# Kernel tuning notes

Hardware: AMD Instinct MI355X
Metric: run time of the kernel (lower is better)

## Reference

```python
import jax, jax.numpy as jnp
import numpy as np

NUM_EMBEDDINGS = 1024
EMBEDDING_DIM = 256
COMMITMENT_COST = 0.25
B, C, T = 16, 256, 4096


def setup_inputs() -> dict:
    key = jax.random.key(0)
    k_in, k_cb = jax.random.split(key)
    inputs = jax.random.normal(k_in, (B, C, T), dtype=jnp.float32)
    # matches nn.Embedding init uniform_(-1/K, 1/K)
    codebook = jax.random.uniform(
        k_cb, (NUM_EMBEDDINGS, EMBEDDING_DIM), dtype=jnp.float32,
        minval=-1.0 / NUM_EMBEDDINGS, maxval=1.0 / NUM_EMBEDDINGS)
    return {"inputs": inputs, "codebook": codebook}


def reference(inputs, codebook):
    # inputs: [B, C, T] -> [B, T, C] (channel-last), eval mode (no dead-code swap)
    x = jnp.transpose(inputs, (0, 2, 1))            # [B, T, C]
    flat = x.reshape(-1, EMBEDDING_DIM)             # [N, D]
    distances = (jnp.sum(flat * flat, axis=1, keepdims=True)
                 + jnp.sum(codebook * codebook, axis=1)
                 - 2.0 * jnp.matmul(flat, codebook.T))   # [N, K]
    encoding_indices = jnp.argmin(distances, axis=1)     # [N]
    quantized = codebook[encoding_indices].reshape(x.shape)  # [B, T, C]
    sg = jax.lax.stop_gradient
    e_latent_loss = jnp.mean(jnp.square(sg(quantized) - x))
    q_latent_loss = jnp.mean(jnp.square(quantized - sg(x)))
    vq_loss = e_latent_loss + COMMITMENT_COST * q_latent_loss
    quantized_st = x + sg(quantized - x)                 # straight-through
    quantized_st = jnp.transpose(quantized_st, (0, 2, 1))  # back to [B, C, T]
    indices = encoding_indices.reshape(B, T)
    return quantized_st, vq_loss, indices
```

## Files before the change

### kernel.cpp

```cpp
#include <hip/hip_runtime.h>
#include <stdint.h>

#define DIMS 256
#define NT 4096
#define NROWS 65536
#define THETA 1.5e-4f

typedef float    f32x4_t __attribute__((ext_vector_type(4)));
typedef _Float16 f16x8_t __attribute__((ext_vector_type(8)));
typedef _Float16 f16x4_t __attribute__((ext_vector_type(4)));

#define GLDS16(gsrc, ldst) \
  __builtin_amdgcn_global_load_lds((const __attribute__((address_space(1))) void*)(gsrc), \
      (__attribute__((address_space(3))) void*)(ldst), 16, 0, 0)

__global__ __launch_bounds__(64) void vq_prep(const float* __restrict__ cb,
                                              float* __restrict__ se,
                                              _Float16* __restrict__ cb16){
  __shared__ float sq[256];
  const int k = blockIdx.x;
  const int tid = threadIdx.x;
  float4 v = *(const float4*)(cb + (size_t)k*256 + tid*4);
  f16x4_t p;
  p.x = (_Float16)(v.x * 512.f);
  p.y = (_Float16)(v.y * 512.f);
  p.z = (_Float16)(v.z * 512.f);
  p.w = (_Float16)(v.w * 512.f);
  *(f16x4_t*)(cb16 + (size_t)k*256 + tid*4) = p;
  sq[tid*4+0] = __fmul_rn(v.x, v.x);
  sq[tid*4+1] = __fmul_rn(v.y, v.y);
  sq[tid*4+2] = __fmul_rn(v.z, v.z);
  sq[tid*4+3] = __fmul_rn(v.w, v.w);
  __syncthreads();
  if (tid < 16){
    const int h = tid >> 3, j = tid & 7;
    float r = sq[h*128 + j];
    #pragma unroll
    for (int i = 1; i < 16; ++i) r = __fadd_rn(r, sq[h*128 + j + 8*i]);
    r = __fadd_rn(r, __shfl_xor(r, 1));
    r = __fadd_rn(r, __shfl_xor(r, 2));
    r = __fadd_rn(r, __shfl_xor(r, 4));
    r = __fadd_rn(r, __shfl_xor(r, 8));
    if (tid == 0) se[k] = r;
  }
}


#define AH(r,c)    Ah[(size_t)(r)*264 + (c)]
#define QQ(t,c)    q[(size_t)(t)*260 + (c)]

#define T2I(v, i, v1, i1, v2) { \
  bool lt = (v) < (v1); \
  (v2) = lt ? (v1) : fminf((v2), (v)); \
  (i1) = lt ? (i) : (i1); \
  (v1) = lt ? (v) : (v1); }

#define DECL_T2(M,R) \
  float b1_##M##R = 3.4e38f, b2_##M##R = 3.4e38f; int bi_##M##R = 0x7fffffff;

#define FOLD(M,R) { \
  float v; \
  v = fmaf(a##M##0[R], NEGI, ec0); T2I(v, kb +  0, b1_##M##R, bi_##M##R, b2_##M##R); \
  v = fmaf(a##M##1[R], NEGI, ec1); T2I(v, kb + 16, b1_##M##R, bi_##M##R, b2_##M##R); \
  v = fmaf(a##M##2[R], NEGI, ec2); T2I(v, kb + 32, b1_##M##R, bi_##M##R, b2_##M##R); \
  v = fmaf(a##M##3[R], NEGI, ec3); T2I(v, kb + 48, b1_##M##R, bi_##M##R, b2_##M##R); }

#define MSTEP(MK) { \
  float ov1 = __shfl_xor(v1, MK); int oi1 = __shfl_xor(i1, MK); float ov2 = __shfl_xor(v2, MK); \
  bool tk = ov1 < v1; \
  v2 = tk ? fminf(v1, ov2) : fminf(v2, ov1); \
  i1 = tk ? oi1 : i1; \
  v1 = tk ? ov1 : v1; }

#define MERGE(M,R) { \
  float v1 = b1_##M##R, v2 = b2_##M##R; int i1 = bi_##M##R; \
  MSTEP(1) MSTEP(2) MSTEP(4) MSTEP(8) \
  if (fr == 0) comb[(wr32 + (M)*16 + fq*4 + (R))*4 + wc] = make_float4(v1, __int_as_float(i1), v2, 0.f); }

__global__ __launch_bounds__(512, 1) void vq_scores(
    const float* __restrict__ x, const float* __restrict__ cb,
    const _Float16* __restrict__ cb16, const float* __restrict__ se,
    float* __restrict__ out0, float* __restrict__ out2,
    unsigned* __restrict__ wl, unsigned* __restrict__ cnt, double* __restrict__ accd)
{
  __shared__ __align__(16) char smem[71168];
  _Float16* Ah   = (_Float16*)smem;
  char*     BhRaw= smem + 33792;
  float4*   comb = (float4*)(smem + 66560);
  int*      codeL= (int*)(smem + 70656);
  float*    sxa  = (float*)(smem + 70912);
  float*    q    = (float*)smem;

  const int tid  = threadIdx.x;
  const int lane = tid & 63;
  const int wid  = tid >> 6;
  const int wr   = wid >> 2;
  const int wc   = wid & 3;
  const int fr   = lane & 15;
  const int fq   = lane >> 4;
  const int wr32 = wr * 32;
  const int fq8  = fq * 8;
  const int wcfr = wc*64 + fr;
  const int n0   = blockIdx.x * 64;
  const int bb   = n0 >> 12;
  const int t0   = n0 & 4095;
  const float NEGI = -1.0f/256.0f;

  const int cA = wid*32 + (lane >> 2);
  const int cB = cA + 16;
  const int qA = (lane & 3) ^ ((cA >> 1) & 3);
  const int qB = (lane & 3) ^ ((cB >> 1) & 3);
  const char* cbB = (const char*)cb16;
  const size_t srcA = (size_t)cA*512 + qA*16;
  const size_t srcB = (size_t)cB*512 + qB*16;
  char* dstA = BhRaw + wid*2048;
  char* dstB = dstA + 1024;

  int bOff[4];
  #pragma unroll
  for (int cf = 0; cf < 4; ++cf){
    const int cd = wc*64 + cf*16 + fr;
    bOff[cf] = cd*64 + ((fq ^ ((cd >> 1) & 3)) << 4);
  }

  GLDS16(cbB + srcA, dstA);
  GLDS16(cbB + srcB, dstB);

  {
    const int dup = tid >> 7;
    const int c4  = tid & 7;
    const int tt  = ((tid >> 3) & 15) << 2;
    #pragma unroll
    for (int cc2 = 0; cc2 < 2; ++cc2){
      const int c0 = (dup*2 + cc2) * 32;
      const float* xp = x + ((size_t)(bb*DIMS + c0 + c4*4))*NT + t0 + tt;
      f32x4_t va0 = __builtin_nontemporal_load((const f32x4_t*)(xp));
      f32x4_t va1 = __builtin_nontemporal_load((const f32x4_t*)(xp + NT));
      f32x4_t va2 = __builtin_nontemporal_load((const f32x4_t*)(xp + 2*NT));
      f32x4_t va3 = __builtin_nontemporal_load((const f32x4_t*)(xp + 3*NT));
      #pragma unroll
      for (int j = 0; j < 4; ++j){
        f16x4_t p;
        p.x = (_Float16)(va0[j]);
        p.y = (_Float16)(va1[j]);
        p.z = (_Float16)(va2[j]);
        p.w = (_Float16)(va3[j]);
        *(f16x4_t*)&AH(tt + j, c0 + c4*4) = p;
      }
    }
  }
  comb[(tid >> 2)*4 + (tid & 3)] = make_float4(3.4e38f, __int_as_float(0x7fffffff), 3.4e38f, 0.f);

  const f32x4_t Z = {0.f, 0.f, 0.f, 0.f};
  f32x4_t a00=Z,a01=Z,a02=Z,a03=Z, a10=Z,a11=Z,a12=Z,a13=Z;
  DECL_T2(0,0) DECL_T2(0,1) DECL_T2(0,2) DECL_T2(0,3)
  DECL_T2(1,0) DECL_T2(1,1) DECL_T2(1,2) DECL_T2(1,3)

  __syncthreads();

  for (int p = 0; p < 32; ++p){
    if (p){
      asm volatile("s_waitcnt vmcnt(0)" ::: "memory");
      __builtin_amdgcn_s_barrier();
      asm volatile("" ::: "memory");
    }
    const int nn = p + 1;
    if (nn < 32){
      const char* g = cbB + (size_t)(nn >> 3)*131072 + (size_t)(nn & 7)*64;
      char* d = (nn & 1) ? (dstA + 16384) : dstA;
      GLDS16(g + srcA, d);
      GLDS16(g + srcB, d + 1024);
    }
    {
      const char* bbuf = BhRaw + ((p & 1) << 14);
      f16x8_t bh0 = *(const f16x8_t*)(bbuf + bOff[0]);
      f16x8_t bh1 = *(const f16x8_t*)(bbuf + bOff[1]);
      f16x8_t bh2 = *(const f16x8_t*)(bbuf + bOff[2]);
      f16x8_t bh3 = *(const f16x8_t*)(bbuf + bOff[3]);
      const int cc = p & 7;
      f16x8_t ah0 = *(const f16x8_t*)&AH(wr32 + fr, cc*32 + fq8);
      f16x8_t ah1 = *(const f16x8_t*)&AH(wr32 + 16 + fr, cc*32 + fq8);
      __builtin_amdgcn_s_setprio(1);
      a00 = __builtin_amdgcn_mfma_f32_16x16x32_f16(ah0, bh0, a00, 0, 0, 0);
      a01 = __builtin_amdgcn_mfma_f32_16x16x32_f16(ah0, bh1, a01, 0, 0, 0);
      a02 = __builtin_amdgcn_mfma_f32_16x16x32_f16(ah0, bh2, a02, 0, 0, 0);
      a03 = __builtin_amdgcn_mfma_f32_16x16x32_f16(ah0, bh3, a03, 0, 0, 0);
      a10 = __builtin_amdgcn_mfma_f32_16x16x32_f16(ah1, bh0, a10, 0, 0, 0);
      a11 = __builtin_amdgcn_mfma_f32_16x16x32_f16(ah1, bh1, a11, 0, 0, 0);
      a12 = __builtin_amdgcn_mfma_f32_16x16x32_f16(ah1, bh2, a12, 0, 0, 0);
      a13 = __builtin_amdgcn_mfma_f32_16x16x32_f16(ah1, bh3, a13, 0, 0, 0);
      __builtin_amdgcn_s_setprio(0);
    }
    if ((p & 7) == 7){
      const int kb = (p >> 3)*256 + wcfr;
      const float ec0 = se[kb], ec1 = se[kb+16], ec2 = se[kb+32], ec3 = se[kb+48];
      FOLD(0,0) FOLD(0,1) FOLD(0,2) FOLD(0,3)
      FOLD(1,0) FOLD(1,1) FOLD(1,2) FOLD(1,3)
      a00=Z;a01=Z;a02=Z;a03=Z; a10=Z;a11=Z;a12=Z;a13=Z;
    }
  }

  MERGE(0,0) MERGE(0,1) MERGE(0,2) MERGE(0,3)
  MERGE(1,0) MERGE(1,1) MERGE(1,2) MERGE(1,3)
  __syncthreads();

  {
    const int row = tid >> 3, seg = tid & 7;
    float s = 0.f;
    #pragma unroll
    for (int k = 0; k < 4; ++k){
      f16x8_t hv = *(const f16x8_t*)&AH(row, seg*32 + k*8);
      #pragma unroll
      for (int e = 0; e < 8; ++e){
        float f = (float)hv[e];
        s = fmaf(f, f, s);
      }
    }
    s += __shfl_xor(s, 1);
    s += __shfl_xor(s, 2);
    s += __shfl_xor(s, 4);
    if (seg == 0) sxa[row] = s;
  }
  __syncthreads();

  if (tid < 64){
    float4 pv = comb[tid*4 + 0];
    float v1 = pv.x, v2 = pv.z;
    int   i1 = __float_as_int(pv.y);
    #pragma unroll
    for (int w = 1; w < 4; ++w){
      pv = comb[tid*4 + w];
      bool tk = pv.x < v1;
      v2 = tk ? fminf(v1, pv.z) : fminf(v2, pv.x);
      i1 = tk ? __float_as_int(pv.y) : i1;
      v1 = tk ? pv.x : v1;
    }
    const int r = n0 + tid;
    codeL[tid] = i1;
    out2[r] = (float)i1;
    bool flg = !(v2 - v1 >= THETA);
    if (flg){
      unsigned pos = atomicAdd(cnt, 1u);
      wl[pos] = (unsigned)r;
    }
    double c = flg ? 0.0 : (double)(sxa[tid] + v1);
    #pragma unroll
    for (int m = 1; m < 64; m <<= 1) c += __shfl_xor(c, m);
    if (tid == 0) atomicAdd(accd, c);
  }
  __syncthreads();

  {
    const int r = tid >> 3, seg = tid & 7;
    const float* src = cb + (size_t)codeL[r] * DIMS;
    #pragma unroll
    for (int k = 0; k < 8; ++k){
      float4 v = *(const float4*)(src + k*32 + seg*4);
      *(float4*)&QQ(r, k*32 + seg*4) = v;
    }
  }
  __syncthreads();

  {
    #pragma unroll
    for (int jj = 0; jj < 2; ++jj){
      const int c = wid*32 + jj*16 + (lane >> 2);
      float* dst = out0 + ((size_t)(bb*256 + c))*NT + t0;
      #pragma unroll
      for (int ii = 0; ii < 4; ++ii){
        const int tl = ii*16 + (lane & 3)*4;
        f32x4_t v;
        v[0] = QQ(tl + 0, c);
        v[1] = QQ(tl + 1, c);
        v[2] = QQ(tl + 2, c);
        v[3] = QQ(tl + 3, c);
        __builtin_nontemporal_store(v, (f32x4_t*)(dst + tl));
      }
    }
  }
}

__global__ __launch_bounds__(256) void vq_refine(
    const float* __restrict__ x, const float* __restrict__ cb,
    const float* __restrict__ se,
    const unsigned* __restrict__ wl, const unsigned* __restrict__ cnt,
    float* __restrict__ out2, float* __restrict__ out0, double* __restrict__ accd)
{
  __shared__ float eT[8][1024];
  __shared__ float xs[DIMS][8];
  __shared__ int   rows_s[8];
  __shared__ float sxs[8];
  __shared__ float wv[4][8];
  __shared__ int   wi[4][8];
  __shared__ int   wiF[8];

  const unsigned n = *cnt;
  const unsigned groups = (n + 7u) >> 3;
  const int tid  = threadIdx.x;
  const int lane = tid & 63;
  const int wid  = tid >> 6;

  for (unsigned g = blockIdx.x; g < groups; g += gridDim.x){
    __syncthreads();
    if (tid < 8){
      unsigned e = g*8u + (unsigned)tid;
      rows_s[tid] = (int)wl[e < n ? e : (n - 1u)];
    }
    __syncthreads();
    #pragma unroll
    for (int rep = 0; rep < 8; ++rep){
      int id = rep * 256 + tid;
      int c = id >> 3, r = id & 7;
      int row = rows_s[r];
      xs[c][r] = x[((size_t)((row >> 12)*DIMS + c))*NT + (row & 4095)];
    }
    __syncthreads();
    if (tid < 128){
      const int r = tid >> 4, hj = tid & 15;
      const int h = hj >> 3, j = hj & 7;
      float v0 = xs[h*128 + j][r];
      float s = __fmul_rn(v0, v0);
      #pragma unroll
      for (int i = 1; i < 16; ++i){
        float v = xs[h*128 + j + 8*i][r];
        s = __fadd_rn(s, __fmul_rn(v, v));
      }
      s = __fadd_rn(s, __shfl_xor(s, 1));
      s = __fadd_rn(s, __shfl_xor(s, 2));
      s = __fadd_rn(s, __shfl_xor(s, 4));
      s = __fadd_rn(s, __shfl_xor(s, 8));
      if (hj == 0) sxs[r] = s;
    }

    float s[8][4];
    #pragma unroll
    for (int r = 0; r < 8; ++r)
      #pragma unroll
      for (int u = 0; u < 4; ++u) s[r][u] = 0.f;

    for (int c0 = 0; c0 < DIMS; c0 += 8){
      __syncthreads();
      #pragma unroll
      for (int rep = 0; rep < 8; ++rep){
        int id2 = rep * 256 + tid;
        int k = id2 >> 1, qq = id2 & 1;
        float4 v = *(const float4*)&cb[(size_t)k * DIMS + c0 + qq * 4];
        eT[qq*4 + 0][k] = v.x; eT[qq*4 + 1][k] = v.y;
        eT[qq*4 + 2][k] = v.z; eT[qq*4 + 3][k] = v.w;
      }
      __syncthreads();
      #pragma unroll
      for (int cc = 0; cc < 8; ++cc){
        float4 ev = *(const float4*)&eT[cc][wid*256 + lane*4];
        #pragma unroll
        for (int r = 0; r < 8; ++r){
          float xv = xs[c0 + cc][r];
          s[r][0] = fmaf(xv, ev.x, s[r][0]);
          s[r][1] = fmaf(xv, ev.y, s[r][1]);
          s[r][2] = fmaf(xv, ev.z, s[r][2]);
          s[r][3] = fmaf(xv, ev.w, s[r][3]);
        }
      }
    }

    float4 sek = *(const float4*)&se[wid*256 + lane*4];
    #pragma unroll
    for (int r = 0; r < 8; ++r){
      const float sxv = sxs[r];
      float bv = 3.4e38f; int bi = 0x7fffffff;
      #pragma unroll
      for (int u = 0; u < 4; ++u){
        float d = __fsub_rn(__fadd_rn(sxv, (&sek.x)[u]),
                            __fadd_rn(s[r][u], s[r][u]));
        int k = wid*256 + lane*4 + u;
        if (d < bv || (d == bv && k < bi)) { bv = d; bi = k; }
      }
      #pragma unroll
      for (int m = 1; m < 64; m <<= 1){
        float ov = __shfl_xor(bv, m);
        int   oi = __shfl_xor(bi, m);
        if (ov < bv || (ov == bv && oi < bi)) { bv = ov; bi = oi; }
      }
      if (lane == 0){ wv[wid][r] = bv; wi[wid][r] = bi; }
    }
    __syncthreads();
    if (tid < 8){
      const int r = tid;
      float bv = wv[0][r]; int bi = wi[0][r];
      #pragma unroll
      for (int w = 1; w < 4; ++w){
        float ov = wv[w][r]; int oi = wi[w][r];
        if (ov < bv || (ov == bv && oi < bi)) { bv = ov; bi = oi; }
      }
      wiF[r] = bi;
      if (g*8u + (unsigned)r < n){
        int row = rows_s[r];
        out2[row] = (float)bi;
        atomicAdd(accd, (double)bv);
      }
    }
    __syncthreads();
    #pragma unroll
    for (int r = 0; r < 8; ++r){
      if (g*8u + (unsigned)r < n){
        int row  = rows_s[r];
        int code = wiF[r];
        out0[((size_t)((row >> 12)*256 + tid))*NT + (row & 4095)] = cb[(size_t)code*DIMS + tid];
      }
    }
  }
}

__global__ void vq_final(const double* __restrict__ accd, float* __restrict__ out1){
  *out1 = (float)(1.25 * (*accd) * (1.0 / 16777216.0));
}

extern "C" void kernel_launch(void* const* d_in, const int* in_sizes, int n_in,
                              void* d_out, int out_size, void* d_ws, size_t ws_size,
                              hipStream_t stream)
{
  const float* x  = (const float*)d_in[0];
  const float* cb = (const float*)d_in[1];
  float* out  = (float*)d_out;
  float* out0 = out;
  float* out1 = out + (size_t)16777216;
  float* out2 = out + (size_t)16777217;

  char* ws = (char*)d_ws;
  double*   accd = (double*)(ws + 0);
  unsigned* cnt  = (unsigned*)(ws + 8);
  float*    se   = (float*)(ws + 64);
  unsigned* wl   = (unsigned*)(ws + 4160);
  _Float16* cb16 = (_Float16*)(ws + 266304);

  hipMemsetAsync(d_ws, 0, 16, stream);
  vq_prep  <<<dim3(1024), dim3(64),  0, stream>>>(cb, se, cb16);
  vq_scores<<<dim3(1024), dim3(512), 0, stream>>>(x, cb, cb16, se, out0, out2, wl, cnt, accd);
  vq_refine<<<dim3(512),  dim3(256), 0, stream>>>(x, cb, se, wl, cnt, out2, out0, accd);
  vq_final <<<dim3(1),    dim3(1),   0, stream>>>(accd, out1);
}
```

Baseline: 159.6 us.

## Track top-3 candidates and resolve two-way ties with a cheap pair-refine kernel

```diff
diff --git a/kernel.cpp b/kernel.cpp
--- a/kernel.cpp
+++ b/kernel.cpp
@@ -45,50 +45,68 @@
   }
 }
 
-
 #define AH(r,c)    Ah[(size_t)(r)*264 + (c)]
 #define QQ(t,c)    q[(size_t)(t)*260 + (c)]
 
-#define T2I(v, i, v1, i1, v2) { \
-  bool lt = (v) < (v1); \
-  (v2) = lt ? (v1) : fminf((v2), (v)); \
-  (i1) = lt ? (i) : (i1); \
-  (v1) = lt ? (v) : (v1); }
-
-#define DECL_T2(M,R) \
-  float b1_##M##R = 3.4e38f, b2_##M##R = 3.4e38f; int bi_##M##R = 0x7fffffff;
+#define T3I(v, i, V1, I1, V2, I2, V3) { \
+  bool lt1 = (v) < (V1), lt2 = (v) < (V2), lt3 = (v) < (V3); \
+  (V3) = lt2 ? (V2) : (lt3 ? (v) : (V3)); \
+  (V2) = lt1 ? (V1) : (lt2 ? (v) : (V2)); \
+  (I2) = lt1 ? (I1) : (lt2 ? (i) : (I2)); \
+  (V1) = lt1 ? (v) : (V1); \
+  (I1) = lt1 ? (i) : (I1); }
+
+#define DECL_T3(M,R) \
+  float b1_##M##R = 3.4e38f, b2_##M##R = 3.4e38f, b3_##M##R = 3.4e38f; \
+  int bi_##M##R = 0x7fffffff, bj_##M##R = 0x7fffffff;
 
 #define FOLD(M,R) { \
   float v; \
-  v = fmaf(a##M##0[R], NEGI, ec0); T2I(v, kb +  0, b1_##M##R, bi_##M##R, b2_##M##R); \
-  v = fmaf(a##M##1[R], NEGI, ec1); T2I(v, kb + 16, b1_##M##R, bi_##M##R, b2_##M##R); \
-  v = fmaf(a##M##2[R], NEGI, ec2); T2I(v, kb + 32, b1_##M##R, bi_##M##R, b2_##M##R); \
-  v = fmaf(a##M##3[R], NEGI, ec3); T2I(v, kb + 48, b1_##M##R, bi_##M##R, b2_##M##R); }
-
-#define MSTEP(MK) { \
-  float ov1 = __shfl_xor(v1, MK); int oi1 = __shfl_xor(i1, MK); float ov2 = __shfl_xor(v2, MK); \
-  bool tk = ov1 < v1; \
-  v2 = tk ? fminf(v1, ov2) : fminf(v2, ov1); \
-  i1 = tk ? oi1 : i1; \
-  v1 = tk ? ov1 : v1; }
+  v = fmaf(a##M##0[R], NEGI, ec0); T3I(v, kb +  0, b1_##M##R, bi_##M##R, b2_##M##R, bj_##M##R, b3_##M##R); \
+  v = fmaf(a##M##1[R], NEGI, ec1); T3I(v, kb + 16, b1_##M##R, bi_##M##R, b2_##M##R, bj_##M##R, b3_##M##R); \
+  v = fmaf(a##M##2[R], NEGI, ec2); T3I(v, kb + 32, b1_##M##R, bi_##M##R, b2_##M##R, bj_##M##R, b3_##M##R); \
+  v = fmaf(a##M##3[R], NEGI, ec3); T3I(v, kb + 48, b1_##M##R, bi_##M##R, b2_##M##R, bj_##M##R, b3_##M##R); }
+
+#define M3BODY(ov1, oi1, ov2, oi2, ov3) { \
+  bool t_ = (ov1) < v1; \
+  float m1_ = t_ ? (ov1) : v1;  int j1_ = t_ ? (oi1) : i1; \
+  float xb_ = t_ ? v1 : (ov1);  int jb_ = t_ ? i1 : (oi1); \
+  float a2_ = t_ ? (ov2) : v2;  int ja_ = t_ ? (oi2) : i2; \
+  float a3_ = t_ ? (ov3) : v3; \
+  float bb2_ = t_ ? v2 : (ov2); \
+  bool u_ = a2_ < xb_; \
+  float m2_ = u_ ? a2_ : xb_; int j2_ = u_ ? ja_ : jb_; \
+  float m3_ = u_ ? fminf(a3_, xb_) : fminf(a2_, bb2_); \
+  v1 = m1_; i1 = j1_; v2 = m2_; i2 = j2_; v3 = m3_; }
+
+#define MSTEP3(MK) { \
+  float ov1 = __shfl_xor(v1, MK), ov2 = __shfl_xor(v2, MK), ov3 = __shfl_xor(v3, MK); \
+  int oi1 = __shfl_xor(i1, MK), oi2 = __shfl_xor(i2, MK); \
+  M3BODY(ov1, oi1, ov2, oi2, ov3) }
 
 #define MERGE(M,R) { \
-  float v1 = b1_##M##R, v2 = b2_##M##R; int i1 = bi_##M##R; \
-  MSTEP(1) MSTEP(2) MSTEP(4) MSTEP(8) \
-  if (fr == 0) comb[(wr32 + (M)*16 + fq*4 + (R))*4 + wc] = make_float4(v1, __int_as_float(i1), v2, 0.f); }
+  float v1 = b1_##M##R, v2 = b2_##M##R, v3 = b3_##M##R; \
+  int i1 = bi_##M##R, i2 = bj_##M##R; \
+  MSTEP3(1) MSTEP3(2) MSTEP3(4) MSTEP3(8) \
+  if (fr == 0){ \
+    comb4[(wr32 + (M)*16 + fq*4 + (R))*4 + wc] = make_float4(v1, __int_as_float(i1), v2, __int_as_float(i2)); \
+    comb3[(wr32 + (M)*16 + fq*4 + (R))*4 + wc] = v3; } }
 
 __global__ __launch_bounds__(512, 1) void vq_scores(
     const float* __restrict__ x, const float* __restrict__ cb,
     const _Float16* __restrict__ cb16, const float* __restrict__ se,
     float* __restrict__ out0, float* __restrict__ out2,
-    unsigned* __restrict__ wl, unsigned* __restrict__ cnt, double* __restrict__ accd)
+    unsigned* __restrict__ wlB, uint4* __restrict__ wlA,
+    unsigned* __restrict__ cntB, unsigned* __restrict__ cntA,
+    double* __restrict__ accd)
 {
-  __shared__ __align__(16) char smem[71168];
+  __shared__ __align__(16) char smem[72192];
   _Float16* Ah   = (_Float16*)smem;
   char*     BhRaw= smem + 33792;
-  float4*   comb = (float4*)(smem + 66560);
-  int*      codeL= (int*)(smem + 70656);
-  float*    sxa  = (float*)(smem + 70912);
+  float4*   comb4= (float4*)(smem + 66560);
+  float*    comb3= (float*)(smem + 70656);
+  int*      codeL= (int*)(smem + 71680);
+  float*    sxa  = (float*)(smem + 71936);
   float*    q    = (float*)smem;
 
   const int tid  = threadIdx.x;
@@ -149,12 +167,11 @@
       }
     }
   }
-  comb[(tid >> 2)*4 + (tid & 3)] = make_float4(3.4e38f, __int_as_float(0x7fffffff), 3.4e38f, 0.f);
 
   const f32x4_t Z = {0.f, 0.f, 0.f, 0.f};
   f32x4_t a00=Z,a01=Z,a02=Z,a03=Z, a10=Z,a11=Z,a12=Z,a13=Z;
-  DECL_T2(0,0) DECL_T2(0,1) DECL_T2(0,2) DECL_T2(0,3)
-  DECL_T2(1,0) DECL_T2(1,1) DECL_T2(1,2) DECL_T2(1,3)
+  DECL_T3(0,0) DECL_T3(0,1) DECL_T3(0,2) DECL_T3(0,3)
+  DECL_T3(1,0) DECL_T3(1,1) DECL_T3(1,2) DECL_T3(1,3)
 
   __syncthreads();
 
@@ -224,26 +241,28 @@
   __syncthreads();
 
   if (tid < 64){
-    float4 pv = comb[tid*4 + 0];
-    float v1 = pv.x, v2 = pv.z;
-    int   i1 = __float_as_int(pv.y);
+    float4 p4 = comb4[tid*4 + 0];
+    float v1 = p4.x, v2 = p4.z, v3 = comb3[tid*4 + 0];
+    int   i1 = __float_as_int(p4.y), i2 = __float_as_int(p4.w);
     #pragma unroll
     for (int w = 1; w < 4; ++w){
-      pv = comb[tid*4 + w];
-      bool tk = pv.x < v1;
-      v2 = tk ? fminf(v1, pv.z) : fminf(v2, pv.x);
-      i1 = tk ? __float_as_int(pv.y) : i1;
-      v1 = tk ? pv.x : v1;
+      float4 o4 = comb4[tid*4 + w];
+      float ov3 = comb3[tid*4 + w];
+      M3BODY(o4.x, __float_as_int(o4.y), o4.z, __float_as_int(o4.w), ov3)
     }
     const int r = n0 + tid;
     codeL[tid] = i1;
     out2[r] = (float)i1;
-    bool flg = !(v2 - v1 >= THETA);
-    if (flg){
-      unsigned pos = atomicAdd(cnt, 1u);
-      wl[pos] = (unsigned)r;
-    }
-    double c = flg ? 0.0 : (double)(sxa[tid] + v1);
+    bool f2 = !(v2 - v1 >= THETA);
+    bool f3 = !(v3 - v1 >= THETA);
+    if (f3){
+      unsigned pos = atomicAdd(cntB, 1u);
+      wlB[pos] = (unsigned)r;
+    } else if (f2){
+      unsigned pos = atomicAdd(cntA, 1u);
+      wlA[pos] = make_uint4((unsigned)r, (unsigned)i1, (unsigned)i2, 0u);
+    }
+    double c = (f2 | f3) ? 0.0 : (double)(sxa[tid] + v1);
     #pragma unroll
     for (int m = 1; m < 64; m <<= 1) c += __shfl_xor(c, m);
     if (tid == 0) atomicAdd(accd, c);
@@ -276,6 +295,58 @@
         v[3] = QQ(tl + 3, c);
         __builtin_nontemporal_store(v, (f32x4_t*)(dst + tl));
       }
+    }
+  }
+}
+
+__global__ __launch_bounds__(256) void vq_pair(
+    const float* __restrict__ x, const float* __restrict__ cb,
+    const float* __restrict__ se,
+    const uint4* __restrict__ wlA, const unsigned* __restrict__ cntA,
+    float* __restrict__ out2, float* __restrict__ out0, double* __restrict__ accd)
+{
+  const unsigned n = *cntA;
+  for (unsigned e = blockIdx.x*256 + threadIdx.x; e < n; e += gridDim.x*256){
+    uint4 w = wlA[e];
+    const int row = (int)w.x, i1 = (int)w.y, i2 = (int)w.z;
+    const int b = row >> 12, t = row & 4095;
+    const float* xp = x + (size_t)b*DIMS*NT + t;
+    float r[16];
+    #pragma unroll
+    for (int j = 0; j < 16; ++j) r[j] = 0.f;
+    #pragma unroll
+    for (int c = 0; c < 256; ++c){
+      float xv = xp[(size_t)c * NT];
+      r[((c >> 7) << 3) | (c & 7)] =
+        __fadd_rn(r[((c >> 7) << 3) | (c & 7)], __fmul_rn(xv, xv));
+    }
+    float h0 = __fadd_rn(__fadd_rn(__fadd_rn(r[0],r[1]), __fadd_rn(r[2],r[3])),
+                         __fadd_rn(__fadd_rn(r[4],r[5]), __fadd_rn(r[6],r[7])));
+    float h1 = __fadd_rn(__fadd_rn(__fadd_rn(r[8],r[9]), __fadd_rn(r[10],r[11])),
+                         __fadd_rn(__fadd_rn(r[12],r[13]), __fadd_rn(r[14],r[15])));
+    float sx = __fadd_rn(h0, h1);
+    const float* c1 = cb + (size_t)i1 * DIMS;
+    const float* c2 = cb + (size_t)i2 * DIMS;
+    float m1 = 0.f, m2 = 0.f;
+    #pragma unroll 8
+    for (int c = 0; c < 256; ++c){
+      float xv = xp[(size_t)c * NT];
+      m1 = fmaf(xv, c1[c], m1);
+      m2 = fmaf(xv, c2[c], m2);
+    }
+    float d1 = __fsub_rn(__fadd_rn(sx, se[i1]), __fadd_rn(m1, m1));
+    float d2 = __fsub_rn(__fadd_rn(sx, se[i2]), __fadd_rn(m2, m2));
+    int win; float dw;
+    if (d1 < d2){ win = i1; dw = d1; }
+    else if (d2 < d1){ win = i2; dw = d2; }
+    else { win = (i1 < i2) ? i1 : i2; dw = d1; }
+    out2[row] = (float)win;
+    atomicAdd(accd, (double)dw);
+    if (win != i1){
+      const float* cw = cb + (size_t)win * DIMS;
+      #pragma unroll 8
+      for (int c = 0; c < 256; ++c)
+        out0[((size_t)(b*DIMS + c))*NT + t] = cw[c];
     }
   }
 }
@@ -428,14 +499,18 @@
 
   char* ws = (char*)d_ws;
   double*   accd = (double*)(ws + 0);
-  unsigned* cnt  = (unsigned*)(ws + 8);
+  unsigned* cntA = (unsigned*)(ws + 8);
+  unsigned* cntB = (unsigned*)(ws + 12);
   float*    se   = (float*)(ws + 64);
-  unsigned* wl   = (unsigned*)(ws + 4160);
-  _Float16* cb16 = (_Float16*)(ws + 266304);
+  unsigned* wlB  = (unsigned*)(ws + 4160);
+  uint4*    wlA  = (uint4*)(ws + 69696);
+  _Float16* cb16 = (_Float16*)(ws + 331840);
 
   hipMemsetAsync(d_ws, 0, 16, stream);
   vq_prep  <<<dim3(1024), dim3(64),  0, stream>>>(cb, se, cb16);
-  vq_scores<<<dim3(1024), dim3(512), 0, stream>>>(x, cb, cb16, se, out0, out2, wl, cnt, accd);
-  vq_refine<<<dim3(512),  dim3(256), 0, stream>>>(x, cb, se, wl, cnt, out2, out0, accd);
+  vq_scores<<<dim3(1024), dim3(512), 0, stream>>>(x, cb, cb16, se, out0, out2,
+                                                  wlB, wlA, cntB, cntA, accd);
+  vq_pair  <<<dim3(32),   dim3(256), 0, stream>>>(x, cb, se, wlA, cntA, out2, out0, accd);
+  vq_refine<<<dim3(64),   dim3(256), 0, stream>>>(x, cb, se, wlB, cntB, out2, out0, accd);
   vq_final <<<dim3(1),    dim3(1),   0, stream>>>(accd, out1);
 }
```

Result: slower. 374.6 us (+134.8%).
